# Optimization experiments

Hardware: AMD Instinct MI355X
Metric: run time of the kernel (lower is better)

## Reference

```python
import jax, jax.numpy as jnp
import numpy as np

HIDDEN = 1024
N_HEAD = 16
HEAD_DIM = HIDDEN // N_HEAD

def setup_inputs() -> dict:
    key = jax.random.key(0)
    ks = jax.random.split(key, 5)
    B, T = 2, 2048
    s_in = 1.0 / np.sqrt(HIDDEN)
    return {
        "x": jax.random.normal(ks[0], (B, T, HIDDEN), dtype=jnp.float32),
        "w_attn": jax.random.normal(ks[1], (HIDDEN, 3 * HIDDEN), dtype=jnp.float32) * s_in,
        "b_attn": jnp.zeros((3 * HIDDEN,), dtype=jnp.float32),
        "w_proj": jax.random.normal(ks[2], (HIDDEN, HIDDEN), dtype=jnp.float32) * s_in,
        "b_proj": jnp.zeros((HIDDEN,), dtype=jnp.float32),
    }

def reference(x, w_attn, b_attn, w_proj, b_proj):
    B, T, C = x.shape
    qkv = x @ w_attn + b_attn  # (B, T, 3C)
    q, k, v = jnp.split(qkv, 3, axis=-1)
    # (B, H, T, D)
    q = q.reshape(B, T, N_HEAD, HEAD_DIM).transpose(0, 2, 1, 3)
    k = k.reshape(B, T, N_HEAD, HEAD_DIM).transpose(0, 2, 1, 3)
    v = v.reshape(B, T, N_HEAD, HEAD_DIM).transpose(0, 2, 1, 3)
    scale = 1.0 / np.sqrt(HEAD_DIM).astype(np.float32)
    attn = jnp.einsum('bhqd,bhkd->bhqk', q, k) * scale
    causal = jnp.tril(jnp.ones((T, T), dtype=bool))
    attn = jnp.where(causal[None, None], attn, -jnp.inf)
    attn = jax.nn.softmax(attn, axis=-1)
    out = jnp.einsum('bhqk,bhkd->bhqd', attn, v)
    out = out.transpose(0, 2, 1, 3).reshape(B, T, C)
    return out @ w_proj + b_proj
```

## Files before the change

### kernel.cpp

```cpp
#include <hip/hip_runtime.h>
#include <stdint.h>

#define T_SEQ 2048
#define NB 2
#define NH 16
#define HD 64
#define HID 1024
#define MTOK (NB * T_SEQ)

typedef float f32x4 __attribute__((ext_vector_type(4)));
typedef float f32x16 __attribute__((ext_vector_type(16)));
typedef short bf16x8 __attribute__((ext_vector_type(8)));
typedef unsigned short u16;
typedef unsigned int u32;

#define QSCALE 0.1803368801f

__device__ __forceinline__ u16 f2bf(float f) {
  union { float f; uint32_t u; } v; v.f = f;
  return (u16)((v.u + 0x7fffu + ((v.u >> 16) & 1u)) >> 16);
}

__device__ __forceinline__ void gl_lds16(const void* g, void* l) {
  __builtin_amdgcn_global_load_lds(
      (const __attribute__((address_space(1))) unsigned int*)g,
      (__attribute__((address_space(3))) unsigned int*)l, 16, 0, 0);
}

__global__ void convert_k(const float* __restrict__ in, u16* __restrict__ out, int n4) {
  int i = blockIdx.x * blockDim.x + threadIdx.x;
  int stride = gridDim.x * blockDim.x;
  for (; i < n4; i += stride) {
    float4 f = ((const float4*)in)[i];
    ushort4 o;
    o.x = f2bf(f.x); o.y = f2bf(f.y); o.z = f2bf(f.z); o.w = f2bf(f.w);
    ((ushort4*)out)[i] = o;
  }
}

__global__ void transpose_k(const float* __restrict__ in, u16* __restrict__ out, int R, int C) {
  __shared__ float tile[32][33];
  int c0 = blockIdx.x * 32, r0 = blockIdx.y * 32;
  int tx = threadIdx.x, ty = threadIdx.y;
#pragma unroll
  for (int i = 0; i < 32; i += 8)
    tile[ty + i][tx] = in[(size_t)(r0 + ty + i) * C + c0 + tx];
  __syncthreads();
#pragma unroll
  for (int i = 0; i < 32; i += 8)
    out[(size_t)(c0 + ty + i) * R + r0 + tx] = f2bf(tile[tx][ty + i]);
}

template <int MODE>
__global__ __launch_bounds__(512, 6)
void gemm_k(const u16* __restrict__ A, const u16* __restrict__ Bt,
            const float* __restrict__ bias,
            u16* __restrict__ q, u16* __restrict__ kk, u16* __restrict__ v,
            float* __restrict__ outf) {
  __shared__ __align__(16) char lds[49152];
  const int tid = threadIdx.x, wid = tid >> 6, lane = tid & 63;
  const int m0 = blockIdx.y * 128, n0 = blockIdx.x * 128;
  const int wm = (wid >> 2) * 64, wn = (wid & 3) * 32;

  f32x4 acc[4][2];
  const f32x4 z = {0.f, 0.f, 0.f, 0.f};
#pragma unroll
  for (int mi = 0; mi < 4; ++mi)
#pragma unroll
    for (int ni = 0; ni < 2; ++ni) acc[mi][ni] = z;

  const int srow = tid >> 2;
  const int scb = (tid & 3) << 4;
  const int scsrc = (scb ^ ((srow & 3) << 4)) >> 1;
  const int rA = lane & 15;
  const int kbyte = (lane >> 4) << 4;

#define GSTAGE(tt_, bi_)                                                      \
  do {                                                                        \
    const int k0_ = (tt_) << 5;                                               \
    char* ab_ = lds + (bi_) * 16384;                                          \
    char* bb_ = ab_ + 8192;                                                   \
    gl_lds16(A + (size_t)(m0 + srow) * HID + k0_ + scsrc, ab_ + wid * 1024);  \
    gl_lds16(Bt + (size_t)(n0 + srow) * HID + k0_ + scsrc, bb_ + wid * 1024); \
  } while (0)

  GSTAGE(0, 0);
  GSTAGE(1, 1);
  GSTAGE(2, 2);

  int cur = 0;
  for (int tt = 0; tt < 32; ++tt) {
    if (tt < 30)       asm volatile("s_waitcnt vmcnt(4)" ::: "memory");
    else if (tt == 30) asm volatile("s_waitcnt vmcnt(2)" ::: "memory");
    else               asm volatile("s_waitcnt vmcnt(0)" ::: "memory");
    __builtin_amdgcn_s_barrier();
    __builtin_amdgcn_sched_barrier(0);

    const char* ab = lds + cur * 16384;
    const char* bb = ab + 8192;
    bf16x8 a[4], b[2];
#pragma unroll
    for (int mi = 0; mi < 4; ++mi) {
      const int row = wm + mi * 16 + rA;
      a[mi] = *(const bf16x8*)(ab + row * 64 + (kbyte ^ ((row & 3) << 4)));
    }
#pragma unroll
    for (int ni = 0; ni < 2; ++ni) {
      const int row = wn + ni * 16 + rA;
      b[ni] = *(const bf16x8*)(bb + row * 64 + (kbyte ^ ((row & 3) << 4)));
    }
#pragma unroll
    for (int mi = 0; mi < 4; ++mi)
#pragma unroll
      for (int ni = 0; ni < 2; ++ni)
        acc[mi][ni] = __builtin_amdgcn_mfma_f32_16x16x32_bf16(a[mi], b[ni], acc[mi][ni], 0, 0, 0);

    __builtin_amdgcn_s_barrier();
    __builtin_amdgcn_sched_barrier(0);
    if (tt + 3 < 32) GSTAGE(tt + 3, cur);
    cur = (cur == 2) ? 0 : cur + 1;
  }
#undef GSTAGE

  const int coll = lane & 15, rowl = (lane >> 4) << 2;
#pragma unroll
  for (int mi = 0; mi < 4; ++mi) {
#pragma unroll
    for (int ni = 0; ni < 2; ++ni) {
      const int n = n0 + wn + ni * 16 + coll;
      const float bv = bias[n];
#pragma unroll
      for (int r = 0; r < 4; ++r) {
        const int m = m0 + wm + mi * 16 + rowl + r;
        float val = acc[mi][ni][r] + bv;
        if (MODE == 0) {
          const int reg = n >> 10, c = n & 1023, h = c >> 6, d = c & 63;
          const int bb2 = m >> 11, t = m & 2047;
          if (reg == 0) q[((size_t)(bb2 * NH + h) * T_SEQ + t) * HD + d] = f2bf(val * QSCALE);
          else if (reg == 1) kk[((size_t)(bb2 * NH + h) * T_SEQ + t) * HD + d] = f2bf(val);
          else v[((size_t)(bb2 * NH + h) * HD + d) * T_SEQ + t] = f2bf(val);
        } else {
          outf[(size_t)m * HID + n] = val;
        }
      }
    }
  }
}

__global__ __launch_bounds__(512, 4)
void attn_k(const u16* __restrict__ Q, const u16* __restrict__ K,
            const u16* __restrict__ Vt, u16* __restrict__ AO) {
  __shared__ __align__(16) char lds[65536];
  const int tid = threadIdx.x;
  const int lane = tid & 63;
  const int wid = tid >> 6;
  const int qsub = wid & 3, par = wid >> 2;
  const int bid = blockIdx.x;
  const int halfg = bid >> 8, r8 = bid & 255;
  const int bh = (r8 & 7) * 4 + ((r8 >> 3) & 3);
  const int lvl = r8 >> 5;
  const int qb = halfg ? lvl : (15 - lvl);
  const int q0 = qb * 128;
  const int ql = lane & 31, h = lane >> 5;
  const bool hi = (h != 0);

  const u16* Qg = Q + (size_t)bh * T_SEQ * HD;
  const u16* Kg = K + (size_t)bh * T_SEQ * HD;
  const u16* Vg = Vt + (size_t)bh * T_SEQ * HD;

  const int q0w = q0 + qsub * 32;
  const int dq = 2 * qb + (qsub >> 1);

  bf16x8 qf[4];
#pragma unroll
  for (int s = 0; s < 4; ++s)
    qf[s] = *(const bf16x8*)(Qg + (size_t)(q0w + ql) * HD + s * 16 + h * 8);

  f32x16 ot0, ot1;
#pragma unroll
  for (int i = 0; i < 16; ++i) { ot0[i] = 0.f; ot1[i] = 0.f; }
  float m = -3.0e38f, l = 0.f;

  const int srow = tid >> 3;
  const int scb = (tid & 7) << 4;
  const int sc0 = (scb ^ ((srow & 7) << 4)) >> 1;

  const int nsup = qb + 1;

#define STAGE(tt_)                                                            \
  do {                                                                        \
    const int kv0_ = (tt_) << 6;                                              \
    gl_lds16(Kg + (size_t)(kv0_ + srow) * HD + sc0,                           \
             lds + (((tt_) & 3) << 13) + wid * 1024);                         \
    gl_lds16(Vg + (size_t)srow * T_SEQ + kv0_ + sc0,                          \
             lds + 32768 + (((tt_) & 3) << 13) + wid * 1024);                 \
  } while (0)

  STAGE(0);
  STAGE(1);

  for (int ss = 0; ss < nsup; ++ss) {
    if (ss + 1 < nsup) {
      STAGE(2 * ss + 2);
      STAGE(2 * ss + 3);
      asm volatile("s_waitcnt vmcnt(4)" ::: "memory");
    } else {
      asm volatile("s_waitcnt vmcnt(0)" ::: "memory");
    }
    __builtin_amdgcn_s_barrier();
    __builtin_amdgcn_sched_barrier(0);

    const int tt = 2 * ss + par;
    if (tt <= dq) {
      const int kv0 = tt << 6;
      const char* kb = lds + ((tt & 3) << 13);
      const char* vb = lds + 32768 + ((tt & 3) << 13);
      f32x16 s0, s1;
#pragma unroll
      for (int i = 0; i < 16; ++i) { s0[i] = 0.f; s1[i] = 0.f; }
#pragma unroll
      for (int s = 0; s < 4; ++s) {
        const int cb = 32 * s + 16 * h;
        const int r0 = ql, r1 = 32 + ql;
        bf16x8 kf0 = *(const bf16x8*)(kb + r0 * 128 + (cb ^ ((r0 & 7) << 4)));
        bf16x8 kf1 = *(const bf16x8*)(kb + r1 * 128 + (cb ^ ((r1 & 7) << 4)));
        s0 = __builtin_amdgcn_mfma_f32_32x32x16_bf16(kf0, qf[s], s0, 0, 0, 0);
        s1 = __builtin_amdgcn_mfma_f32_32x32x16_bf16(kf1, qf[s], s1, 0, 0, 0);
      }
      if (tt == dq) {
        const int qg = q0w + ql;
#pragma unroll
        for (int r = 0; r < 16; ++r) {
          const int kvl = (r & 3) + 8 * (r >> 2) + 4 * h;
          if (kv0 + kvl > qg) s0[r] = -3.0e38f;
          if (kv0 + 32 + kvl > qg) s1[r] = -3.0e38f;
        }
      }
      float mx[16];
#pragma unroll
      for (int i = 0; i < 16; ++i) mx[i] = fmaxf(s0[i], s1[i]);
#pragma unroll
      for (int d = 8; d; d >>= 1)
#pragma unroll
        for (int i = 0; i < d; ++i) mx[i] = fmaxf(mx[i], mx[i + d]);
      const float tm = fmaxf(mx[0], __shfl_xor(mx[0], 32, 64));
      if (!__all(tm <= m + 4.0f)) {
        const float mnew = fmaxf(m, tm);
        const float fold = __builtin_amdgcn_exp2f(m - mnew);
        m = mnew;
        l *= fold;
#pragma unroll
        for (int i = 0; i < 16; ++i) { ot0[i] *= fold; ot1[i] *= fold; }
      }
#pragma unroll
      for (int i = 0; i < 16; ++i) {
        s0[i] = __builtin_amdgcn_exp2f(s0[i] - m);
        s1[i] = __builtin_amdgcn_exp2f(s1[i] - m);
      }
      float sm[16];
#pragma unroll
      for (int i = 0; i < 16; ++i) sm[i] = s0[i] + s1[i];
#pragma unroll
      for (int d = 8; d; d >>= 1)
#pragma unroll
        for (int i = 0; i < d; ++i) sm[i] += sm[i + d];
      l += sm[0] + __shfl_xor(sm[0], 32, 64);

      u32 w0[8], w1[8];
#pragma unroll
      for (int mm = 0; mm < 8; ++mm) {
        asm("v_cvt_pk_bf16_f32 %0, %1, %2" : "=v"(w0[mm]) : "v"(s0[2 * mm]), "v"(s0[2 * mm + 1]));
        asm("v_cvt_pk_bf16_f32 %0, %1, %2" : "=v"(w1[mm]) : "v"(s1[2 * mm]), "v"(s1[2 * mm + 1]));
      }
#pragma unroll
      for (int sb = 0; sb < 2; ++sb) {
#pragma unroll
        for (int t = 0; t < 2; ++t) {
          u32 a0 = sb ? w1[4 * t]     : w0[4 * t];
          u32 a1 = sb ? w1[4 * t + 1] : w0[4 * t + 1];
          u32 a2 = sb ? w1[4 * t + 2] : w0[4 * t + 2];
          u32 a3 = sb ? w1[4 * t + 3] : w0[4 * t + 3];
          u32 snd0 = hi ? a0 : a2;
          u32 snd1 = hi ? a1 : a3;
          u32 own0 = hi ? a2 : a0;
          u32 own1 = hi ? a3 : a1;
          u32 p0 = __shfl_xor(snd0, 32, 64);
          u32 p1 = __shfl_xor(snd1, 32, 64);
          union { u32 u[4]; bf16x8 v; } fr;
          fr.u[0] = hi ? p0 : own0;
          fr.u[1] = hi ? p1 : own1;
          fr.u[2] = hi ? own0 : p0;
          fr.u[3] = hi ? own1 : p1;
          const int s = sb * 2 + t;
          const int cb = 32 * s + 16 * h;
          const int r0 = ql, r1 = 32 + ql;
          bf16x8 vf0 = *(const bf16x8*)(vb + r0 * 128 + (cb ^ ((r0 & 7) << 4)));
          bf16x8 vf1 = *(const bf16x8*)(vb + r1 * 128 + (cb ^ ((r1 & 7) << 4)));
          ot0 = __builtin_amdgcn_mfma_f32_32x32x16_bf16(vf0, fr.v, ot0, 0, 0, 0);
          ot1 = __builtin_amdgcn_mfma_f32_32x32x16_bf16(vf1, fr.v, ot1, 0, 0, 0);
        }
      }
    }
    __builtin_amdgcn_s_barrier();
    __builtin_amdgcn_sched_barrier(0);
  }
#undef STAGE

  float* R = (float*)(lds + qsub * 8448);
  if (par == 1) {
#pragma unroll
    for (int r = 0; r < 16; ++r) {
      const int dl = (r & 3) + 8 * (r >> 2) + 4 * h;
      R[ql * 66 + dl] = ot0[r];
      R[ql * 66 + 32 + dl] = ot1[r];
    }
    if (!hi) { R[ql * 66 + 64] = m; R[ql * 66 + 65] = l; }
  }
  __builtin_amdgcn_s_barrier();
  if (par == 1) return;

  const float m2 = R[ql * 66 + 64];
  const float l2 = R[ql * 66 + 65];
  const float M = fmaxf(m, m2);
  const float c1 = __builtin_amdgcn_exp2f(m - M);
  const float c2 = __builtin_amdgcn_exp2f(m2 - M);
  const float L = c1 * l + c2 * l2;
  const float inv = 1.0f / L;
  float of0[16], of1[16];
#pragma unroll
  for (int r = 0; r < 16; ++r) {
    const int dl = (r & 3) + 8 * (r >> 2) + 4 * h;
    of0[r] = (c1 * ot0[r] + c2 * R[ql * 66 + dl]) * inv;
    of1[r] = (c1 * ot1[r] + c2 * R[ql * 66 + 32 + dl]) * inv;
  }
  asm volatile("s_waitcnt lgkmcnt(0)" ::: "memory");
  __builtin_amdgcn_sched_barrier(0);

  float* E = (float*)(lds + qsub * 8448);
#pragma unroll
  for (int r = 0; r < 16; ++r) {
    const int dl = (r & 3) + 8 * (r >> 2) + 4 * h;
    E[dl * 33 + ql] = of0[r];
    E[(dl + 32) * 33 + ql] = of1[r];
  }
  asm volatile("s_waitcnt lgkmcnt(0)" ::: "memory");
  __builtin_amdgcn_sched_barrier(0);
  const int bb = bh >> 4, hh = bh & 15;
  const int r2 = lane >> 3;
  const int c8 = (lane & 7) * 8;
#pragma unroll
  for (int g = 0; g < 4; ++g) {
    const int qrow = g * 8 + r2;
    union { u16 a[8]; bf16x8 v; } ov;
#pragma unroll
    for (int j = 0; j < 8; ++j) ov.a[j] = f2bf(E[(c8 + j) * 33 + qrow]);
    *(bf16x8*)(AO + (size_t)(bb * T_SEQ + q0 + qsub * 32 + qrow) * HID + hh * HD + c8) = ov.v;
  }
}

extern "C" void kernel_launch(void* const* d_in, const int* in_sizes, int n_in,
                              void* d_out, int out_size, void* d_ws, size_t ws_size,
                              hipStream_t stream) {
  const float* x      = (const float*)d_in[0];
  const float* w_attn = (const float*)d_in[1];
  const float* b_attn = (const float*)d_in[2];
  const float* w_proj = (const float*)d_in[3];
  const float* b_proj = (const float*)d_in[4];
  float* out = (float*)d_out;

  char* ws = (char*)d_ws;
  u16* xb   = (u16*)(ws);
  u16* wabT = (u16*)(ws + (size_t)(8  << 20));
  u16* wpbT = (u16*)(ws + (size_t)(14 << 20));
  u16* q    = (u16*)(ws + (size_t)(16 << 20));
  u16* k    = (u16*)(ws + (size_t)(24 << 20));
  u16* v    = (u16*)(ws + (size_t)(32 << 20));
  u16* ao   = (u16*)(ws + (size_t)(40 << 20));

  convert_k<<<dim3(1024), dim3(256), 0, stream>>>(x, xb, MTOK * HID / 4);
  transpose_k<<<dim3(96, 32), dim3(32, 8), 0, stream>>>(w_attn, wabT, HID, 3 * HID);
  transpose_k<<<dim3(32, 32), dim3(32, 8), 0, stream>>>(w_proj, wpbT, HID, HID);
  gemm_k<0><<<dim3(24, 32), dim3(512), 0, stream>>>(xb, wabT, b_attn, q, k, v, nullptr);
  attn_k<<<dim3(512), dim3(512), 0, stream>>>(q, k, v, ao);
  gemm_k<1><<<dim3(8, 32), dim3(512), 0, stream>>>(ao, wpbT, b_proj, nullptr, nullptr, nullptr, out);
}
```

Baseline: 107.5 us.

## Replace QKV GEMM with 256x256-tile kernel using phased LDS pipeline

```diff
diff --git a/kernel.cpp b/kernel.cpp
--- a/kernel.cpp
+++ b/kernel.cpp
@@ -49,6 +49,121 @@
 #pragma unroll
   for (int i = 0; i < 32; i += 8)
     out[(size_t)(c0 + ty + i) * R + r0 + tx] = f2bf(tile[tx][ty + i]);
+}
+
+__global__ __launch_bounds__(512, 2)
+void gemm256_k(const u16* __restrict__ A, const u16* __restrict__ Bt,
+               const float* __restrict__ bias,
+               u16* __restrict__ q, u16* __restrict__ kk, u16* __restrict__ v) {
+  __shared__ __align__(16) char lds[131072];
+  const int tid = threadIdx.x, wid = tid >> 6, lane = tid & 63;
+  const int m0 = blockIdx.y * 256, n0 = blockIdx.x * 256;
+  const int ahalf = wid >> 2;
+  const int bsel = wid & 3;
+  const int bhalf = bsel >> 1, nl0 = (bsel & 1) * 64;
+  const int rA = lane & 15, kb16 = (lane >> 4) << 4;
+  const int lr = lane >> 3;
+  const int scsrc = ((((lane & 7) << 4) ^ (lr << 4)) >> 1);
+  const int w8lr = wid * 8 + lr;
+
+  f32x4 acc[8][4];
+  const f32x4 z = {0.f, 0.f, 0.f, 0.f};
+#pragma unroll
+  for (int mi = 0; mi < 8; ++mi)
+#pragma unroll
+    for (int ni = 0; ni < 4; ++ni) acc[mi][ni] = z;
+  bf16x8 bfr[4][2];
+  bf16x8 afr[2][2];
+
+#define SLOT(kt) (((kt) & 1) << 16)
+#define ST_A(kt, h) do { \
+    const u16* s_ = A + (size_t)(m0 + (h) * 128 + w8lr) * HID + (kt) * 64 + scsrc; \
+    char* d_ = lds + SLOT(kt) + (h) * 16384 + wid * 1024; \
+    gl_lds16(s_, d_); \
+    gl_lds16(s_ + (size_t)64 * HID, d_ + 8192); \
+  } while (0)
+#define ST_B(kt, h) do { \
+    const u16* s_ = Bt + (size_t)(n0 + (h) * 128 + w8lr) * HID + (kt) * 64 + scsrc; \
+    char* d_ = lds + SLOT(kt) + 32768 + (h) * 16384 + wid * 1024; \
+    gl_lds16(s_, d_); \
+    gl_lds16(s_ + (size_t)64 * HID, d_ + 8192); \
+  } while (0)
+#define LDA(m2, mi, ks) { const int r_ = (mi) * 16 + rA; \
+    afr[m2][ks] = *(const bf16x8*)(lds + sb + ahalf * 16384 + r_ * 128 + \
+                                   ((((ks) * 64) + kb16) ^ ((r_ & 7) << 4))); }
+#define LDB(ni, ks) { const int r_ = nl0 + (ni) * 16 + rA; \
+    bfr[ni][ks] = *(const bf16x8*)(lds + sb + 32768 + bhalf * 16384 + r_ * 128 + \
+                                   ((((ks) * 64) + kb16) ^ ((r_ & 7) << 4))); }
+#define VMW(n) asm volatile("s_waitcnt vmcnt(" #n ")" ::: "memory")
+#define PH_MFMA(qq) \
+    __builtin_amdgcn_s_setprio(1); \
+    _Pragma("unroll") \
+    for (int ks = 0; ks < 2; ++ks) \
+      _Pragma("unroll") \
+      for (int ni = 0; ni < 4; ++ni) { \
+        acc[2*(qq)][ni]   = __builtin_amdgcn_mfma_f32_16x16x32_bf16(afr[0][ks], bfr[ni][ks], acc[2*(qq)][ni], 0, 0, 0); \
+        acc[2*(qq)+1][ni] = __builtin_amdgcn_mfma_f32_16x16x32_bf16(afr[1][ks], bfr[ni][ks], acc[2*(qq)+1][ni], 0, 0, 0); \
+      } \
+    __builtin_amdgcn_s_setprio(0);
+#define PHASE(qq, WAIT, STG) do { \
+    WAIT; \
+    __builtin_amdgcn_s_barrier(); \
+    asm volatile("" ::: "memory"); \
+    STG; \
+    LDA(0, 2*(qq), 0); LDA(0, 2*(qq), 1); LDA(1, 2*(qq)+1, 0); LDA(1, 2*(qq)+1, 1); \
+    if ((qq) == 0) { LDB(0,0); LDB(0,1); LDB(1,0); LDB(1,1); LDB(2,0); LDB(2,1); LDB(3,0); LDB(3,1); } \
+    PH_MFMA(qq); \
+  } while (0)
+
+  ST_B(0, 0); ST_B(0, 1); ST_A(0, 0); ST_A(0, 1); ST_B(1, 0); ST_B(1, 1);
+
+  for (int i = 0; i < 8; ++i) {
+    const int kte = 2 * i, kto = 2 * i + 1;
+    const bool pf = (i < 7);
+    {
+      const int sb = SLOT(kte);
+      PHASE(0, VMW(4), { ST_A(kto, 0); });
+      PHASE(1, ((void)0), { ST_A(kto, 1); });
+      PHASE(2, ((void)0), { if (pf) ST_B(kte + 2, 0); });
+      PHASE(3, ((void)0), { if (pf) ST_B(kte + 2, 1); });
+    }
+    {
+      const int sb = SLOT(kto);
+      PHASE(0, { if (pf) { VMW(4); } else { VMW(0); } }, { if (pf) ST_A(kte + 2, 0); });
+      PHASE(1, ((void)0), { if (pf) ST_A(kte + 2, 1); });
+      PHASE(2, ((void)0), { if (pf) ST_B(kto + 2, 0); });
+      PHASE(3, ((void)0), { if (pf) ST_B(kto + 2, 1); });
+    }
+  }
+#undef PHASE
+#undef PH_MFMA
+#undef VMW
+#undef LDB
+#undef LDA
+#undef ST_B
+#undef ST_A
+#undef SLOT
+
+  const int coll = lane & 15, rowl = (lane >> 4) << 2;
+  const int wmg = (wid >> 2) * 128, wng = (wid & 3) * 64;
+#pragma unroll
+  for (int mi = 0; mi < 8; ++mi) {
+#pragma unroll
+    for (int ni = 0; ni < 4; ++ni) {
+      const int n = n0 + wng + ni * 16 + coll;
+      const float bv = bias[n];
+#pragma unroll
+      for (int r = 0; r < 4; ++r) {
+        const int m = m0 + wmg + mi * 16 + rowl + r;
+        const float val = acc[mi][ni][r] + bv;
+        const int reg = n >> 10, c = n & 1023, h = c >> 6, d = c & 63;
+        const int bb2 = m >> 11, t = m & 2047;
+        if (reg == 0) q[((size_t)(bb2 * NH + h) * T_SEQ + t) * HD + d] = f2bf(val * QSCALE);
+        else if (reg == 1) kk[((size_t)(bb2 * NH + h) * T_SEQ + t) * HD + d] = f2bf(val);
+        else v[((size_t)(bb2 * NH + h) * HD + d) * T_SEQ + t] = f2bf(val);
+      }
+    }
+  }
 }
 
 template <int MODE>
@@ -380,7 +495,7 @@
   convert_k<<<dim3(1024), dim3(256), 0, stream>>>(x, xb, MTOK * HID / 4);
   transpose_k<<<dim3(96, 32), dim3(32, 8), 0, stream>>>(w_attn, wabT, HID, 3 * HID);
   transpose_k<<<dim3(32, 32), dim3(32, 8), 0, stream>>>(w_proj, wpbT, HID, HID);
-  gemm_k<0><<<dim3(24, 32), dim3(512), 0, stream>>>(xb, wabT, b_attn, q, k, v, nullptr);
+  gemm256_k<<<dim3(12, 16), dim3(512), 0, stream>>>(xb, wabT, b_attn, q, k, v);
   attn_k<<<dim3(512), dim3(512), 0, stream>>>(q, k, v, ao);
   gemm_k<1><<<dim3(8, 32), dim3(512), 0, stream>>>(ao, wpbT, b_proj, nullptr, nullptr, nullptr, out);
 }
```

After: 118.9 us. 10.6% more time.
